# Kernel optimization log

Measured on AMD Instinct MI355X. Metric: run time of the kernel, lower is better.

The kernel has to match this reference:

```python
import jax, jax.numpy as jnp
import numpy as np

K_HIDDEN = 512
N_POS = 24
N_COLOR = 6
EPS = 1e-5


def setup_inputs() -> dict:
    key = jax.random.key(0)
    k1, k2 = jax.random.split(key)
    B = 1024
    x = jax.random.normal(k1, (B, N_POS, N_COLOR * K_HIDDEN), dtype=jnp.float32)
    # kaiming-uniform-ish scale for the (k_out, k_in, 2) weight
    fan_in = K_HIDDEN * 2
    bound = float(np.sqrt(6.0 / fan_in))
    conv_weight = jax.random.uniform(k2, (K_HIDDEN, K_HIDDEN, 2), dtype=jnp.float32,
                                     minval=-bound, maxval=bound)
    conv_bias = jnp.zeros((K_HIDDEN,), dtype=jnp.float32)
    norm_weight = jnp.ones((K_HIDDEN,), dtype=jnp.float32)
    norm_bias = jnp.zeros((K_HIDDEN,), dtype=jnp.float32)
    return {"x": x, "conv_weight": conv_weight, "conv_bias": conv_bias,
            "norm_weight": norm_weight, "norm_bias": norm_bias}


def _color_layernorm(x, gamma, beta):
    # x: (B, 24, 6*k); normalize over the full channel axis, affine tied per block of 6
    mean = jnp.mean(x, axis=-1, keepdims=True)
    var = jnp.mean(jnp.square(x - mean), axis=-1, keepdims=True)  # unbiased=False
    xn = (x - mean) * jax.lax.rsqrt(var + EPS)
    xn = xn.reshape(*x.shape[:-1], K_HIDDEN, N_COLOR)
    xn = xn * gamma[:, None] + beta[:, None]
    return xn.reshape(x.shape)


def _color_conv(x, weight, bias):
    # x: (B, 24, 6*k) -> (B, 24, k, 6)
    B = x.shape[0]
    xr = x.reshape(B, N_POS, K_HIDDEN, N_COLOR)
    alpha = weight[:, :, 0] - weight[:, :, 1]   # (k_out, k_in)
    beta_w = weight[:, :, 1]                    # (k_out, k_in)
    term1 = jnp.einsum('bikd,ok->biod', xr, alpha)      # per-color linear
    x_sum = xr.sum(axis=3)                               # (B, 24, k_in)
    term2 = jnp.einsum('bik,ok->bio', x_sum, beta_w)     # color-sum linear
    out = term1 + term2[..., None] + bias[None, None, :, None]
    return out.reshape(B, N_POS, K_HIDDEN * N_COLOR)


def reference(x, conv_weight, conv_bias, norm_weight, norm_bias):
    h = _color_layernorm(x, norm_weight, norm_bias)
    h = _color_conv(h, conv_weight, conv_bias)
    return x + jax.nn.relu(h)
```

## Files before the change

kernel.cpp:

```cpp
#include <hip/hip_runtime.h>
#include <stdint.h>
#include <stddef.h>

#define KH   512
#define DF   3072
#define EPSF 1e-5f
#define PPB  16
#define ROWS 96
#define TSS  520

typedef __attribute__((ext_vector_type(4))) float f32x4;
typedef __attribute__((ext_vector_type(8))) short bf16x8;

__device__ __forceinline__ unsigned short f2bf(float f) {
  union { float f; unsigned u; } c; c.f = f;
  unsigned u = c.u;
  u += 0x7fffu + ((u >> 16) & 1u);
  return (unsigned short)(u >> 16);
}
__device__ __forceinline__ float bf2f(unsigned short u) {
  union { unsigned u; float f; } c; c.u = ((unsigned)u) << 16;
  return c.f;
}

__global__ __launch_bounds__(256) void prep_w(const float* __restrict__ cw,
                                              const float* __restrict__ cb,
                                              const float* __restrict__ nw,
                                              const float* __restrict__ nb,
                                              unsigned char* __restrict__ wbt,
                                              float* __restrict__ c12) {
  const int o = blockIdx.x;
  const int t = threadIdx.x;
  const int wn = o >> 6, nn = (o >> 4) & 3, co = o & 15;
  float c1 = 0.f, c2 = 0.f;
  for (int k = t; k < KH; k += 256) {
    float w0 = cw[o * 1024 + 2 * k];
    float w1 = cw[o * 1024 + 2 * k + 1];
    float a  = w0 - w1;
    float g  = nw[k], b = nb[k];
    int s = k >> 5, kin = k & 31, h = kin >> 3, e = kin & 7;
    size_t base = (size_t)(((wn * 16 + s) * 4 + nn)) * 1024 + (h * 16 + co) * 16 + e * 2;
    *(unsigned short*)(wbt + base)          = f2bf(a * g);
    *(unsigned short*)(wbt + base + 524288) = f2bf(w1 * g);
    float tt = a + 6.f * w1;
    c1 += tt * b;
    c2 += tt * g;
  }
  #pragma unroll
  for (int off = 32; off >= 1; off >>= 1) {
    c1 += __shfl_xor(c1, off);
    c2 += __shfl_xor(c2, off);
  }
  __shared__ float s1[4], s2[4];
  int wid = t >> 6, lane = t & 63;
  if (lane == 0) { s1[wid] = c1; s2[wid] = c2; }
  __syncthreads();
  if (t == 0) {
    c12[o]      = s1[0] + s1[1] + s1[2] + s1[3] + cb[o];
    c12[KH + o] = s2[0] + s2[1] + s2[2] + s2[3];
  }
}

__global__ __launch_bounds__(1024) void fused_main(
    const float* __restrict__ x,
    const unsigned char* __restrict__ wbt,
    const float* __restrict__ c12,
    float* __restrict__ out)
{
  __shared__ unsigned char As[ROWS * 1024];
  __shared__ unsigned char Sx[PPB * 1024];
  __shared__ float Ts[PPB * TSS];
  __shared__ float st[PPB * 2];

  const int tid  = threadIdx.x;
  const int lane = tid & 63;
  const int wid  = tid >> 6;
  const int wm   = wid >> 3;
  const int wn   = wid & 7;
  const int co   = lane & 15;
  const int h    = lane >> 4;
  const int rvb  = h << 2;
  const int r0   = blockIdx.x * PPB;

  {
    const float* xb = x + (size_t)r0 * DF;
    f32x4 q[12];
    #pragma unroll
    for (int i = 0; i < 12; i++) q[i] = *(const f32x4*)(xb + i * 4096 + tid * 4);

    #pragma unroll
    for (int i = 0; i < 12; i++) {
      int base = i * 4096 + tid * 4;
      int pl   = base / 3072;
      int rem  = base - pl * 3072;
      int k0   = rem / 6;
      int d0   = rem - k0 * 6;
      #pragma unroll
      for (int e = 0; e < 4; e++) {
        int d = d0 + e, k = k0;
        if (d >= 6) { d -= 6; k += 1; }
        int row  = pl * 6 + d;
        int byte = row * 1024 + ((((k >> 3) ^ (row & 7)) << 4)) + (k & 7) * 2;
        *(unsigned short*)(As + byte) = f2bf(q[i][e]);
      }
    }
  }
  __syncthreads();

  {
    float vals[48];
    #pragma unroll
    for (int d = 0; d < 6; d++) {
      int row = wid * 6 + d;
      bf16x8 v = *(const bf16x8*)(As + row * 1024 + ((lane ^ (row & 7)) << 4));
      #pragma unroll
      for (int g = 0; g < 8; g++) vals[d * 8 + g] = bf2f((unsigned short)v[g]);
    }
    float s = 0.f, sq = 0.f;
    #pragma unroll
    for (int i = 0; i < 48; i++) { s += vals[i]; sq += vals[i] * vals[i]; }
    #pragma unroll
    for (int off = 32; off >= 1; off >>= 1) {
      s  += __shfl_xor(s,  off);
      sq += __shfl_xor(sq, off);
    }
    float mean = s * (1.f / 3072.f);
    float var  = sq * (1.f / 3072.f) - mean * mean;
    float rstd = rsqrtf(var + EPSF);
    if (lane == 0) { st[2 * wid] = mean; st[2 * wid + 1] = rstd; }
    bf16x8 sv;
    #pragma unroll
    for (int g = 0; g < 8; g++) {
      float ss = vals[g] + vals[8 + g] + vals[16 + g] + vals[24 + g] +
                 vals[32 + g] + vals[40 + g];
      sv[g] = (short)f2bf(ss);
    }
    *(bf16x8*)(Sx + wid * 1024 + ((lane ^ (wid & 7)) << 4)) = sv;
  }
  __syncthreads();

  f32x4 acc1[3][4];
  #pragma unroll
  for (int m = 0; m < 3; m++)
    #pragma unroll
    for (int n = 0; n < 4; n++) acc1[m][n] = (f32x4){0.f, 0.f, 0.f, 0.f};

  int arow[3], ar7[3];
  #pragma unroll
  for (int m = 0; m < 3; m++) {
    int row = wm * 48 + m * 16 + co;
    arow[m] = row * 1024;  ar7[m] = row & 7;
  }

  {
    const unsigned char* wA = wbt + (size_t)wn * 65536;
    bf16x8 bvc[4], bvn[4];
    #pragma unroll
    for (int n = 0; n < 4; n++)
      bvc[n] = *(const bf16x8*)(wA + n * 1024 + lane * 16);
    #pragma unroll 1
    for (int s = 0; s < 16; s++) {
      if (s < 15) {
        const unsigned char* p = wA + (size_t)(s + 1) * 4096;
        #pragma unroll
        for (int n = 0; n < 4; n++)
          bvn[n] = *(const bf16x8*)(p + n * 1024 + lane * 16);
      }
      int g6 = s * 4 + h;
      bf16x8 af[3];
      #pragma unroll
      for (int m = 0; m < 3; m++)
        af[m] = *(const bf16x8*)(As + arow[m] + ((g6 ^ ar7[m]) << 4));
      #pragma unroll
      for (int m = 0; m < 3; m++)
        #pragma unroll
        for (int n = 0; n < 4; n++)
          acc1[m][n] = __builtin_amdgcn_mfma_f32_16x16x32_bf16(af[m], bvc[n], acc1[m][n], 0, 0, 0);
      #pragma unroll
      for (int n = 0; n < 4; n++) bvc[n] = bvn[n];
    }
  }

  {
    f32x4 acc2[2];
    acc2[0] = (f32x4){0.f, 0.f, 0.f, 0.f};
    acc2[1] = (f32x4){0.f, 0.f, 0.f, 0.f};
    const int sxswz = (co & 7);
    bf16x8 b2c[2], b2n[2];
    #pragma unroll
    for (int n = 0; n < 2; n++) {
      int f = wid * 2 + n;
      b2c[n] = *(const bf16x8*)(wbt + 524288 +
                 (size_t)(((f >> 2) * 16) * 4 + (f & 3)) * 1024 + lane * 16);
    }
    #pragma unroll 1
    for (int s = 0; s < 16; s++) {
      if (s < 15) {
        #pragma unroll
        for (int n = 0; n < 2; n++) {
          int f = wid * 2 + n;
          b2n[n] = *(const bf16x8*)(wbt + 524288 +
                     (size_t)(((f >> 2) * 16 + (s + 1)) * 4 + (f & 3)) * 1024 + lane * 16);
        }
      }
      int g6 = s * 4 + h;
      bf16x8 a2 = *(const bf16x8*)(Sx + co * 1024 + ((g6 ^ sxswz) << 4));
      #pragma unroll
      for (int n = 0; n < 2; n++)
        acc2[n] = __builtin_amdgcn_mfma_f32_16x16x32_bf16(a2, b2c[n], acc2[n], 0, 0, 0);
      b2c[0] = b2n[0]; b2c[1] = b2n[1];
    }
    #pragma unroll
    for (int n = 0; n < 2; n++)
      #pragma unroll
      for (int v = 0; v < 4; v++)
        Ts[(rvb + v) * TSS + wid * 32 + n * 16 + co] = acc2[n][v];
  }
  __syncthreads();

  #pragma unroll
  for (int n = 0; n < 4; n++) {
    const int o    = wn * 64 + n * 16 + co;
    const float C1 = c12[o];
    const float C2 = c12[KH + o];
    const int swzo = o >> 3;
    #pragma unroll
    for (int m = 0; m < 3; m++) {
      #pragma unroll
      for (int v = 0; v < 4; v++) {
        int j  = wm * 48 + m * 16 + rvb + v;
        int pl = j / 6;
        float mean = st[2 * pl], rstd = st[2 * pl + 1];
        float t2   = Ts[pl * TSS + o];
        int byte = j * 1024 + (((swzo ^ (j & 7)) << 4)) + (o & 7) * 2;
        unsigned short rx = *(const unsigned short*)(As + byte);
        float hh = fmaxf(rstd * (acc1[m][n][v] + t2) + C1 - mean * rstd * C2, 0.f);
        *(unsigned short*)(As + byte) = f2bf(bf2f(rx) + hh);
      }
    }
  }
  __syncthreads();

  {
    float* ob = out + (size_t)(r0 + wid) * DF;
    #pragma unroll
    for (int jj = 0; jj < 12; jj++) {
      int c0 = jj * 256 + lane * 4;
      int o0 = c0 / 6;
      int d0 = c0 - o0 * 6;
      f32x4 ov;
      #pragma unroll
      for (int e = 0; e < 4; e++) {
        int d = d0 + e, o = o0;
        if (d >= 6) { d -= 6; o += 1; }
        int row  = wid * 6 + d;
        int byte = row * 1024 + ((((o >> 3) ^ (row & 7)) << 4)) + (o & 7) * 2;
        ov[e] = bf2f(*(const unsigned short*)(As + byte));
      }
      *(f32x4*)(ob + c0) = ov;
    }
  }
}

extern "C" void kernel_launch(void* const* d_in, const int* in_sizes, int n_in,
                              void* d_out, int out_size, void* d_ws, size_t ws_size,
                              hipStream_t stream) {
  (void)n_in; (void)out_size; (void)ws_size;
  const float* x  = (const float*)d_in[0];
  const float* cw = (const float*)d_in[1];
  const float* cb = (const float*)d_in[2];
  const float* nw = (const float*)d_in[3];
  const float* nb = (const float*)d_in[4];
  float* out = (float*)d_out;

  unsigned char* wbt = (unsigned char*)d_ws;
  float* c12 = (float*)((char*)d_ws + (size_t)1024 * 1024);

  prep_w<<<512, 256, 0, stream>>>(cw, cb, nw, nb, wbt, c12);

  const int R = in_sizes[0] / DF;
  fused_main<<<R / PPB, 1024, 0, stream>>>(x, wbt, c12, out);
}
```

Measured before the change: 253.8 us.

## Make fused kernel persistent over six row tiles with prefetched input and direct stores

Each block now loops over six 16-row tiles instead of one. The next tile's x is prefetched into registers while the current tile's epilogue runs, and per-thread constants are hoisted out of the loop. The epilogue writes results straight to global memory instead of staging them in shared memory and running a second store pass. The weight-fragment loop is unrolled by two with double-buffered registers. The aim is to hide global load latency and remove a sync and a shared-memory pass, but the grid shrinks sixfold (R/96 blocks), which may underfill the GPU, and the output writes become strided rather than coalesced.

```diff
diff --git a/kernel.cpp b/kernel.cpp
--- a/kernel.cpp
+++ b/kernel.cpp
@@ -7,9 +7,11 @@
 #define EPSF 1e-5f
 #define PPB  16
 #define ROWS 96
+#define NT   6
 #define TSS  520
 
 typedef __attribute__((ext_vector_type(4))) float f32x4;
+typedef __attribute__((ext_vector_type(2))) float f32x2;
 typedef __attribute__((ext_vector_type(8))) short bf16x8;
 
 __device__ __forceinline__ unsigned short f2bf(float f) {
@@ -61,7 +63,7 @@
   }
 }
 
-__global__ __launch_bounds__(1024) void fused_main(
+__global__ __launch_bounds__(1024, 4) void fused_main(
     const float* __restrict__ x,
     const unsigned char* __restrict__ wbt,
     const float* __restrict__ c12,
@@ -80,13 +82,39 @@
   const int co   = lane & 15;
   const int h    = lane >> 4;
   const int rvb  = h << 2;
-  const int r0   = blockIdx.x * PPB;
-
+
+  float C1r[4], C2r[4];
+  #pragma unroll
+  for (int n = 0; n < 4; n++) {
+    int o = wn * 64 + n * 16 + co;
+    C1r[n] = c12[o];
+    C2r[n] = c12[KH + o];
+  }
+
+  int arow[3], ar7[3];
+  #pragma unroll
+  for (int m = 0; m < 3; m++) {
+    int row = wm * 48 + m * 16 + co;
+    arow[m] = row * 1024;  ar7[m] = row & 7;
+  }
+  const unsigned char* wA = wbt + (size_t)wn * 65536;
+  const unsigned char* wB = wbt + 524288;
+  const int f0 = wid * 2, f1 = wid * 2 + 1;
+  const size_t f0base = (size_t)((f0 >> 2) * 64 + (f0 & 3)) * 1024 + lane * 16;
+  const size_t f1base = (size_t)((f1 >> 2) * 64 + (f1 & 3)) * 1024 + lane * 16;
+  const int sxswz = co & 7;
+
+  const size_t tile0 = (size_t)blockIdx.x * NT * PPB;
+
+  f32x4 p[12];
   {
-    const float* xb = x + (size_t)r0 * DF;
-    f32x4 q[12];
+    const float* xb = x + tile0 * DF;
     #pragma unroll
-    for (int i = 0; i < 12; i++) q[i] = *(const f32x4*)(xb + i * 4096 + tid * 4);
+    for (int i = 0; i < 12; i++) p[i] = *(const f32x4*)(xb + i * 4096 + tid * 4);
+  }
+
+  for (int t = 0; t < NT; ++t) {
+    const size_t r0 = tile0 + (size_t)t * PPB;
 
     #pragma unroll
     for (int i = 0; i < 12; i++) {
@@ -101,164 +129,185 @@
         if (d >= 6) { d -= 6; k += 1; }
         int row  = pl * 6 + d;
         int byte = row * 1024 + ((((k >> 3) ^ (row & 7)) << 4)) + (k & 7) * 2;
-        *(unsigned short*)(As + byte) = f2bf(q[i][e]);
-      }
-    }
-  }
-  __syncthreads();
-
-  {
-    float vals[48];
+        *(unsigned short*)(As + byte) = f2bf(p[i][e]);
+      }
+    }
+    __syncthreads();
+
+    {
+      float vals[48];
+      #pragma unroll
+      for (int d = 0; d < 6; d++) {
+        int row = wid * 6 + d;
+        bf16x8 v = *(const bf16x8*)(As + row * 1024 + ((lane ^ (row & 7)) << 4));
+        #pragma unroll
+        for (int g = 0; g < 8; g++) vals[d * 8 + g] = bf2f((unsigned short)v[g]);
+      }
+      float s = 0.f, sq = 0.f;
+      #pragma unroll
+      for (int i = 0; i < 48; i++) { s += vals[i]; sq += vals[i] * vals[i]; }
+      #pragma unroll
+      for (int off = 32; off >= 1; off >>= 1) {
+        s  += __shfl_xor(s,  off);
+        sq += __shfl_xor(sq, off);
+      }
+      float mean = s * (1.f / 3072.f);
+      float var  = sq * (1.f / 3072.f) - mean * mean;
+      float rstd = rsqrtf(var + EPSF);
+      if (lane == 0) { st[2 * wid] = mean; st[2 * wid + 1] = rstd; }
+      bf16x8 sv;
+      #pragma unroll
+      for (int g = 0; g < 8; g++) {
+        float ss = vals[g] + vals[8 + g] + vals[16 + g] + vals[24 + g] +
+                   vals[32 + g] + vals[40 + g];
+        sv[g] = (short)f2bf(ss);
+      }
+      *(bf16x8*)(Sx + wid * 1024 + ((lane ^ (wid & 7)) << 4)) = sv;
+    }
+    __syncthreads();
+
+    f32x4 acc1[3][4];
     #pragma unroll
-    for (int d = 0; d < 6; d++) {
-      int row = wid * 6 + d;
-      bf16x8 v = *(const bf16x8*)(As + row * 1024 + ((lane ^ (row & 7)) << 4));
-      #pragma unroll
-      for (int g = 0; g < 8; g++) vals[d * 8 + g] = bf2f((unsigned short)v[g]);
-    }
-    float s = 0.f, sq = 0.f;
-    #pragma unroll
-    for (int i = 0; i < 48; i++) { s += vals[i]; sq += vals[i] * vals[i]; }
-    #pragma unroll
-    for (int off = 32; off >= 1; off >>= 1) {
-      s  += __shfl_xor(s,  off);
-      sq += __shfl_xor(sq, off);
-    }
-    float mean = s * (1.f / 3072.f);
-    float var  = sq * (1.f / 3072.f) - mean * mean;
-    float rstd = rsqrtf(var + EPSF);
-    if (lane == 0) { st[2 * wid] = mean; st[2 * wid + 1] = rstd; }
-    bf16x8 sv;
-    #pragma unroll
-    for (int g = 0; g < 8; g++) {
-      float ss = vals[g] + vals[8 + g] + vals[16 + g] + vals[24 + g] +
-                 vals[32 + g] + vals[40 + g];
-      sv[g] = (short)f2bf(ss);
-    }
-    *(bf16x8*)(Sx + wid * 1024 + ((lane ^ (wid & 7)) << 4)) = sv;
-  }
-  __syncthreads();
-
-  f32x4 acc1[3][4];
-  #pragma unroll
-  for (int m = 0; m < 3; m++)
-    #pragma unroll
-    for (int n = 0; n < 4; n++) acc1[m][n] = (f32x4){0.f, 0.f, 0.f, 0.f};
-
-  int arow[3], ar7[3];
-  #pragma unroll
-  for (int m = 0; m < 3; m++) {
-    int row = wm * 48 + m * 16 + co;
-    arow[m] = row * 1024;  ar7[m] = row & 7;
-  }
-
-  {
-    const unsigned char* wA = wbt + (size_t)wn * 65536;
-    bf16x8 bvc[4], bvn[4];
-    #pragma unroll
-    for (int n = 0; n < 4; n++)
-      bvc[n] = *(const bf16x8*)(wA + n * 1024 + lane * 16);
-    #pragma unroll 1
-    for (int s = 0; s < 16; s++) {
-      if (s < 15) {
-        const unsigned char* p = wA + (size_t)(s + 1) * 4096;
+    for (int m = 0; m < 3; m++)
+      #pragma unroll
+      for (int n = 0; n < 4; n++) acc1[m][n] = (f32x4){0.f, 0.f, 0.f, 0.f};
+
+    {
+      bf16x8 bvA[4], bvB[4];
+      #pragma unroll
+      for (int n = 0; n < 4; n++)
+        bvA[n] = *(const bf16x8*)(wA + n * 1024 + lane * 16);
+      #pragma unroll 1
+      for (int s = 0; s < 16; s += 2) {
+        const unsigned char* pn = wA + (size_t)(s + 1) * 4096;
         #pragma unroll
         for (int n = 0; n < 4; n++)
-          bvn[n] = *(const bf16x8*)(p + n * 1024 + lane * 16);
-      }
-      int g6 = s * 4 + h;
-      bf16x8 af[3];
-      #pragma unroll
-      for (int m = 0; m < 3; m++)
-        af[m] = *(const bf16x8*)(As + arow[m] + ((g6 ^ ar7[m]) << 4));
-      #pragma unroll
-      for (int m = 0; m < 3; m++)
+          bvB[n] = *(const bf16x8*)(pn + n * 1024 + lane * 16);
+        {
+          int g6 = s * 4 + h;
+          bf16x8 af[3];
+          #pragma unroll
+          for (int m = 0; m < 3; m++)
+            af[m] = *(const bf16x8*)(As + arow[m] + ((g6 ^ ar7[m]) << 4));
+          #pragma unroll
+          for (int m = 0; m < 3; m++)
+            #pragma unroll
+            for (int n = 0; n < 4; n++)
+              acc1[m][n] = __builtin_amdgcn_mfma_f32_16x16x32_bf16(af[m], bvA[n], acc1[m][n], 0, 0, 0);
+        }
+        if (s + 2 < 16) {
+          const unsigned char* pn2 = wA + (size_t)(s + 2) * 4096;
+          #pragma unroll
+          for (int n = 0; n < 4; n++)
+            bvA[n] = *(const bf16x8*)(pn2 + n * 1024 + lane * 16);
+        }
+        {
+          int g6 = (s + 1) * 4 + h;
+          bf16x8 af[3];
+          #pragma unroll
+          for (int m = 0; m < 3; m++)
+            af[m] = *(const bf16x8*)(As + arow[m] + ((g6 ^ ar7[m]) << 4));
+          #pragma unroll
+          for (int m = 0; m < 3; m++)
+            #pragma unroll
+            for (int n = 0; n < 4; n++)
+              acc1[m][n] = __builtin_amdgcn_mfma_f32_16x16x32_bf16(af[m], bvB[n], acc1[m][n], 0, 0, 0);
+        }
+      }
+    }
+
+    {
+      f32x4 acc2[2];
+      acc2[0] = (f32x4){0.f, 0.f, 0.f, 0.f};
+      acc2[1] = (f32x4){0.f, 0.f, 0.f, 0.f};
+      bf16x8 cA0 = *(const bf16x8*)(wB + f0base);
+      bf16x8 cA1 = *(const bf16x8*)(wB + f1base);
+      bf16x8 cB0, cB1;
+      #pragma unroll 1
+      for (int s = 0; s < 16; s += 2) {
+        cB0 = *(const bf16x8*)(wB + f0base + (size_t)(s + 1) * 4096);
+        cB1 = *(const bf16x8*)(wB + f1base + (size_t)(s + 1) * 4096);
+        {
+          int g6 = s * 4 + h;
+          bf16x8 a2 = *(const bf16x8*)(Sx + co * 1024 + ((g6 ^ sxswz) << 4));
+          acc2[0] = __builtin_amdgcn_mfma_f32_16x16x32_bf16(a2, cA0, acc2[0], 0, 0, 0);
+          acc2[1] = __builtin_amdgcn_mfma_f32_16x16x32_bf16(a2, cA1, acc2[1], 0, 0, 0);
+        }
+        if (s + 2 < 16) {
+          cA0 = *(const bf16x8*)(wB + f0base + (size_t)(s + 2) * 4096);
+          cA1 = *(const bf16x8*)(wB + f1base + (size_t)(s + 2) * 4096);
+        }
+        {
+          int g6 = (s + 1) * 4 + h;
+          bf16x8 a2 = *(const bf16x8*)(Sx + co * 1024 + ((g6 ^ sxswz) << 4));
+          acc2[0] = __builtin_amdgcn_mfma_f32_16x16x32_bf16(a2, cB0, acc2[0], 0, 0, 0);
+          acc2[1] = __builtin_amdgcn_mfma_f32_16x16x32_bf16(a2, cB1, acc2[1], 0, 0, 0);
+        }
+      }
+      #pragma unroll
+      for (int n = 0; n < 2; n++)
         #pragma unroll
-        for (int n = 0; n < 4; n++)
-          acc1[m][n] = __builtin_amdgcn_mfma_f32_16x16x32_bf16(af[m], bvc[n], acc1[m][n], 0, 0, 0);
-      #pragma unroll
-      for (int n = 0; n < 4; n++) bvc[n] = bvn[n];
-    }
-  }
-
-  {
-    f32x4 acc2[2];
-    acc2[0] = (f32x4){0.f, 0.f, 0.f, 0.f};
-    acc2[1] = (f32x4){0.f, 0.f, 0.f, 0.f};
-    const int sxswz = (co & 7);
-    bf16x8 b2c[2], b2n[2];
+        for (int v = 0; v < 4; v++)
+          Ts[(rvb + v) * TSS + wid * 32 + n * 16 + co] = acc2[n][v];
+    }
+    __syncthreads();
+
+    if (t + 1 < NT) {
+      const float* xb = x + (r0 + PPB) * DF;
+      #pragma unroll
+      for (int i = 0; i < 12; i++) p[i] = *(const f32x4*)(xb + i * 4096 + tid * 4);
+      __builtin_amdgcn_sched_barrier(0);
+    }
+
     #pragma unroll
-    for (int n = 0; n < 2; n++) {
-      int f = wid * 2 + n;
-      b2c[n] = *(const bf16x8*)(wbt + 524288 +
-                 (size_t)(((f >> 2) * 16) * 4 + (f & 3)) * 1024 + lane * 16);
-    }
-    #pragma unroll 1
-    for (int s = 0; s < 16; s++) {
-      if (s < 15) {
-        #pragma unroll
-        for (int n = 0; n < 2; n++) {
-          int f = wid * 2 + n;
-          b2n[n] = *(const bf16x8*)(wbt + 524288 +
-                     (size_t)(((f >> 2) * 16 + (s + 1)) * 4 + (f & 3)) * 1024 + lane * 16);
-        }
-      }
-      int g6 = s * 4 + h;
-      bf16x8 a2 = *(const bf16x8*)(Sx + co * 1024 + ((g6 ^ sxswz) << 4));
-      #pragma unroll
-      for (int n = 0; n < 2; n++)
-        acc2[n] = __builtin_amdgcn_mfma_f32_16x16x32_bf16(a2, b2c[n], acc2[n], 0, 0, 0);
-      b2c[0] = b2n[0]; b2c[1] = b2n[1];
-    }
-    #pragma unroll
-    for (int n = 0; n < 2; n++)
-      #pragma unroll
-      for (int v = 0; v < 4; v++)
-        Ts[(rvb + v) * TSS + wid * 32 + n * 16 + co] = acc2[n][v];
-  }
-  __syncthreads();
-
-  #pragma unroll
-  for (int n = 0; n < 4; n++) {
-    const int o    = wn * 64 + n * 16 + co;
-    const float C1 = c12[o];
-    const float C2 = c12[KH + o];
-    const int swzo = o >> 3;
-    #pragma unroll
-    for (int m = 0; m < 3; m++) {
-      #pragma unroll
-      for (int v = 0; v < 4; v++) {
-        int j  = wm * 48 + m * 16 + rvb + v;
-        int pl = j / 6;
-        float mean = st[2 * pl], rstd = st[2 * pl + 1];
-        float t2   = Ts[pl * TSS + o];
-        int byte = j * 1024 + (((swzo ^ (j & 7)) << 4)) + (o & 7) * 2;
-        unsigned short rx = *(const unsigned short*)(As + byte);
-        float hh = fmaxf(rstd * (acc1[m][n][v] + t2) + C1 - mean * rstd * C2, 0.f);
-        *(unsigned short*)(As + byte) = f2bf(bf2f(rx) + hh);
-      }
-    }
-  }
-  __syncthreads();
-
-  {
-    float* ob = out + (size_t)(r0 + wid) * DF;
-    #pragma unroll
-    for (int jj = 0; jj < 12; jj++) {
-      int c0 = jj * 256 + lane * 4;
-      int o0 = c0 / 6;
-      int d0 = c0 - o0 * 6;
-      f32x4 ov;
-      #pragma unroll
-      for (int e = 0; e < 4; e++) {
-        int d = d0 + e, o = o0;
-        if (d >= 6) { d -= 6; o += 1; }
-        int row  = wid * 6 + d;
-        int byte = row * 1024 + ((((o >> 3) ^ (row & 7)) << 4)) + (o & 7) * 2;
-        ov[e] = bf2f(*(const unsigned short*)(As + byte));
-      }
-      *(f32x4*)(ob + c0) = ov;
-    }
+    for (int n = 0; n < 4; n++) {
+      const int o = wn * 64 + n * 16 + co;
+      const int swzo = o >> 3;
+      const int ob2 = (o & 7) * 2;
+      #pragma unroll
+      for (int m = 0; m < 3; m++) {
+        int j0  = wm * 48 + m * 16 + rvb;
+        int pl0 = j0 / 6;
+        int d0  = j0 - pl0 * 6;
+        float mean0 = st[2 * pl0], rstd0 = st[2 * pl0 + 1];
+        float t20   = Ts[pl0 * TSS + o];
+        float cc0   = C1r[n] - mean0 * rstd0 * C2r[n];
+        if (d0 < 3) {
+          f32x4 ov;
+          #pragma unroll
+          for (int v = 0; v < 4; v++) {
+            int j = j0 + v;
+            unsigned short rx = *(const unsigned short*)(
+                As + j * 1024 + ((swzo ^ (j & 7)) << 4) + ob2);
+            ov[v] = bf2f(rx) + fmaxf(rstd0 * (acc1[m][n][v] + t20) + cc0, 0.f);
+          }
+          *(f32x4*)(out + (r0 + pl0) * DF + o * 6 + d0) = ov;
+        } else {
+          int pl1 = pl0 + 1;
+          float mean1 = st[2 * pl1], rstd1 = st[2 * pl1 + 1];
+          float t21   = Ts[pl1 * TSS + o];
+          float cc1   = C1r[n] - mean1 * rstd1 * C2r[n];
+          f32x2 o0, o1;
+          #pragma unroll
+          for (int v = 0; v < 2; v++) {
+            int j = j0 + v;
+            unsigned short rx = *(const unsigned short*)(
+                As + j * 1024 + ((swzo ^ (j & 7)) << 4) + ob2);
+            o0[v] = bf2f(rx) + fmaxf(rstd0 * (acc1[m][n][v] + t20) + cc0, 0.f);
+          }
+          #pragma unroll
+          for (int v = 2; v < 4; v++) {
+            int j = j0 + v;
+            unsigned short rx = *(const unsigned short*)(
+                As + j * 1024 + ((swzo ^ (j & 7)) << 4) + ob2);
+            o1[v - 2] = bf2f(rx) + fmaxf(rstd1 * (acc1[m][n][v] + t21) + cc1, 0.f);
+          }
+          *(f32x2*)(out + (r0 + pl0) * DF + o * 6 + 4) = o0;
+          *(f32x2*)(out + (r0 + pl1) * DF + o * 6)     = o1;
+        }
+      }
+    }
+    __syncthreads();
   }
 }
 
@@ -279,5 +328,5 @@
   prep_w<<<512, 256, 0, stream>>>(cw, cb, nw, nb, wbt, c12);
 
   const int R = in_sizes[0] / DF;
-  fused_main<<<R / PPB, 1024, 0, stream>>>(x, wbt, c12, out);
-}
+  fused_main<<<R / (PPB * NT), 1024, 0, stream>>>(x, wbt, c12, out);
+}
```

Measured after the change: 772.2 us. +204.2%, slower.
